# Kernel tuning notes

Measured on AMD Instinct MI355X. Metric: run time of the kernel, lower is better.

## Reference

```python
import jax, jax.numpy as jnp
import numpy as np

MIN_SCORE = 0.3       # min_score_threshold
NMS_THRESHOLD = 0.3   # nms_threshold
MAX_OUT = 256         # fixed output padding (jit-compatible replacement for dynamic K)


def _cxcywh_to_xyxy(b):
    cx, cy, w, h = b[..., 0], b[..., 1], b[..., 2], b[..., 3]
    half_w, half_h = w * 0.5, h * 0.5
    return jnp.stack([cx - half_w, cy - half_h, cx + half_w, cy + half_h], axis=-1)


def _pairwise_iou(a, b):
    # a: [N,4], b: [M,4] in xyxy
    lt = jnp.maximum(a[:, None, :2], b[None, :, :2])
    rb = jnp.minimum(a[:, None, 2:], b[None, :, 2:])
    wh = jnp.clip(rb - lt, 0.0)
    inter = wh[..., 0] * wh[..., 1]
    area_a = (a[:, 2] - a[:, 0]) * (a[:, 3] - a[:, 1])
    area_b = (b[:, 2] - b[:, 0]) * (b[:, 3] - b[:, 1])
    return inter / (area_a[:, None] + area_b[None, :] - inter + 1e-9)


def setup_inputs() -> dict:
    key = jax.random.key(0)
    k1, k2 = jax.random.split(key)
    N, n_coords = 8192, 16
    score = jax.random.uniform(k1, (N, 1), dtype=jnp.float32)
    box = jax.random.uniform(k2, (N, n_coords), dtype=jnp.float32)
    return {"score": score, "box": box}


def reference(score, box):
    # score: [N,1], box: [N,n_coords]; single class (n_classes==1, cls=None)
    s = score[:, 0]
    valid = s >= MIN_SCORE                      # score mask applied before NMS
    order = jnp.argsort(-s)                     # score-descending (batched_nms order)
    s_s = s[order]
    v_s = valid[order]
    box_s = box[order]
    bbox = _cxcywh_to_xyxy(box_s[:, :4]).astype(jnp.float32)
    iou = _pairwise_iou(bbox, bbox)             # [N,N]
    N = s.shape[0]

    def body(kept, i):
        # suppressed if overlaps any already-kept (higher-score) box
        suppressed = jnp.any(kept & (iou[:, i] > NMS_THRESHOLD))
        keep_i = v_s[i] & jnp.logical_not(suppressed)
        return kept.at[i].set(keep_i), None

    kept, _ = jax.lax.scan(body, jnp.zeros((N,), dtype=bool), jnp.arange(N))

    # compact kept detections to the front, preserving score order (stable sort)
    comp = jnp.argsort(jnp.where(kept, 0, 1), stable=True)[:MAX_OUT]
    out_valid = kept[comp]                      # [MAX_OUT]
    score_out = jnp.where(out_valid[:, None], s_s[comp][:, None], 0.0)   # [MAX_OUT,1]
    box_out = jnp.where(out_valid[:, None], box_s[comp], 0.0)            # [MAX_OUT,n_coords]
    return score_out, box_out, out_valid
```

## Files before the change

### kernel.cpp

```cpp
#include <hip/hip_runtime.h>
#include <stdint.h>

typedef unsigned long long u64;

#define N 8192
#define NW 128
#define MAX_OUT 256
#define MASK_BYTES ((size_t)N * NW * 8)


__global__ __launch_bounds__(256)
void build_keys_kernel(const float* __restrict__ score, u64* __restrict__ keys,
                       int* __restrict__ rank, int* __restrict__ nvalid) {
    int i = blockIdx.x * 256 + threadIdx.x;
    float s = score[i];
    uint32_t b = __float_as_uint(s);
    keys[i] = ((u64)(~b) << 32) | (uint32_t)i;
    rank[i] = 0;
    int c = (s >= 0.3f) ? 1 : 0;
    for (int off = 32; off; off >>= 1) c += __shfl_down(c, off);
    __shared__ int part[4];
    if ((threadIdx.x & 63) == 0) part[threadIdx.x >> 6] = c;
    __syncthreads();
    if (threadIdx.x == 0) atomicAdd(nvalid, part[0] + part[1] + part[2] + part[3]);
}

__global__ __launch_bounds__(256)
void rank_kernel(const u64* __restrict__ keys, int* __restrict__ rank) {
    __shared__ u64 kj[1024];
    const int tid = threadIdx.x;
    const int jbase = blockIdx.y * 1024;
    for (int t = tid; t < 1024; t += 256) kj[t] = keys[jbase + t];
    __syncthreads();
    const int i = blockIdx.x * 256 + tid;
    const u64 ki = keys[i];
    int c = 0;
    #pragma unroll 8
    for (int j = 0; j < 1024; ++j) c += (kj[j] < ki) ? 1 : 0;
    atomicAdd(&rank[i], c);
}

__global__ __launch_bounds__(256)
void scatter_kernel(const float* __restrict__ score, const float* __restrict__ box,
                    const int* __restrict__ rank, int* __restrict__ order,
                    float* __restrict__ s_s, float4* __restrict__ bbox,
                    float* __restrict__ area) {
    int i = blockIdx.x * 256 + threadIdx.x;
    int r = rank[i];
    float s = score[i];
    order[r] = i;
    s_s[r] = s;
    float4 cb = ((const float4*)box)[i * 4];
    float hw = cb.z * 0.5f, hh = cb.w * 0.5f;
    float x0 = cb.x - hw, y0 = cb.y - hh, x1 = cb.x + hw, y1 = cb.y + hh;
    bbox[r] = make_float4(x0, y0, x1, y1);
    area[r] = (x1 - x0) * (y1 - y0);
}

__global__ __launch_bounds__(256)
void mask_kernel(const float4* __restrict__ bbox, const float* __restrict__ area,
                 const int* __restrict__ nvalid_p, u64* __restrict__ mask) {
    const int w = blockIdx.x;
    const int i = blockIdx.y * 256 + threadIdx.x;
    __shared__ float4 jb[64];
    __shared__ float  ja[64];
    if (threadIdx.x < 64) {
        jb[threadIdx.x] = bbox[w * 64 + threadIdx.x];
        ja[threadIdx.x] = area[w * 64 + threadIdx.x];
    }
    __syncthreads();
    const int nv = *nvalid_p;
    if (i >= nv) return;
    if (w < (i >> 6)) return;
    float4 a = bbox[i];
    float  aa = area[i];
    u64 bits = 0;
    #pragma unroll 8
    for (int jj = 0; jj < 64; ++jj) {
        float4 b = jb[jj];
        float lx = fmaxf(a.x, b.x), ly = fmaxf(a.y, b.y);
        float rx = fminf(a.z, b.z), ry = fminf(a.w, b.w);
        float ww = fmaxf(rx - lx, 0.0f), hh = fmaxf(ry - ly, 0.0f);
        float inter = ww * hh;
        float denom = ((aa + ja[jj]) - inter) + 1e-9f;
        float iou = inter / denom;
        bits |= ((u64)(iou > 0.3f)) << jj;
    }
    mask[(size_t)i * NW + w] = bits;
}


struct Pipe { u64 col, s1, s2, g0, g1, g2, g3; };

__device__ __forceinline__ u64 wave_or64(u64 v) {
    unsigned lo = (unsigned)v, hi = (unsigned)(v >> 32);
    #pragma unroll
    for (int off = 1; off < 64; off <<= 1) {
        lo |= (unsigned)__shfl_xor((int)lo, off, 64);
        hi |= (unsigned)__shfl_xor((int)hi, off, 64);
    }
    return ((u64)hi << 32) | (u64)lo;
}

__global__ __launch_bounds__(64)
void nms_kernel(const u64* __restrict__ mask, const float* __restrict__ s_s,
                const int* __restrict__ order, const float* __restrict__ box,
                const int* __restrict__ nvalid_p, float* __restrict__ out) {
    const int lane = threadIdx.x;
    const int nv = *nvalid_p;
    const int nblk = (nv + 63) >> 6;
    __shared__ int kpos[MAX_OUT];
    int kcount = 0;
    u64 s1m = 0, s2m = 0, s2m_old = 0;

    Pipe A, B;
    A.col = A.s1 = A.s2 = A.g0 = A.g1 = A.g2 = A.g3 = 0;
    B.col = B.s1 = B.s2 = B.g0 = B.g1 = B.g2 = B.g3 = 0;
    if (nblk > 0) {
        const u64* r = mask + (size_t)lane * NW;
        A.col = r[0];
        if (nblk > 1) A.s1 = r[1];
        if (nblk > 2) A.s2 = r[2];
    }
    if (nblk > 1) {
        const u64* r = mask + (size_t)(64 + lane) * NW;
        B.col = r[1];
        if (nblk > 2) B.s1 = r[2];
        if (nblk > 3) B.s2 = r[3];
    }

    auto step = [&](int b, Pipe& P) -> bool {
        u64 col = P.col, s1v = P.s1, s2v = P.s2;
        u64 x = P.g0 | P.g1 | P.g2 | P.g3 | s1m | s2m_old;
        const int b2 = b + 2;
        P.col = P.s1 = P.s2 = P.g0 = P.g1 = P.g2 = P.g3 = 0;
        if (b2 < nblk) {
            const u64* r = mask + (size_t)((b2 << 6) + lane) * NW;
            P.col = r[b2];
            if (b2 + 1 < nblk) P.s1 = r[b2 + 1];
            if (b2 + 2 < nblk) P.s2 = r[b2 + 2];
            const int kc = kcount;
            if (lane < kc)       P.g0 = mask[(size_t)kpos[lane]       * NW + b2];
            if (lane +  64 < kc) P.g1 = mask[(size_t)kpos[lane +  64] * NW + b2];
            if (lane + 128 < kc) P.g2 = mask[(size_t)kpos[lane + 128] * NW + b2];
            if (lane + 192 < kc) P.g3 = mask[(size_t)kpos[lane + 192] * NW + b2];
        }
        u64 rw = wave_or64(x);
        const int base = b << 6;
        const int rem = nv - base;
        u64 validm = (rem >= 64) ? ~0ull : ((1ull << rem) - 1ull);
        u64 todo = validm & ~rw;
        u64 km = 0;
        while (todo) {
            int l = (int)__builtin_ctzll(todo);
            u64 row_l = __ballot(((col >> l) & 1ull) != 0);
            if (lane == 0) kpos[kcount] = base + l;
            km |= (1ull << l);
            kcount++;
            todo &= ~row_l;
            todo &= ~(1ull << l);
            if (kcount >= MAX_OUT) break;
        }
        u64 keepm = ((km >> lane) & 1ull) ? ~0ull : 0ull;
        s2m_old = s2m;
        s2m = s2v & keepm;
        s1m = s1v & keepm;
        return kcount < MAX_OUT;
    };

    bool run = true;
    for (int b = 0; run && b < nblk; b += 2) {
        run = step(b, A);
        if (run && b + 1 < nblk) run = step(b + 1, B);
    }

    __syncthreads();
    float* out_score = out;
    float* out_box   = out + MAX_OUT;
    float* out_valid = out + MAX_OUT + MAX_OUT * 16;
    const float4* box4 = (const float4*)box;
    float4* ob4 = (float4*)out_box;
    for (int t = lane; t < MAX_OUT; t += 64) {
        if (t < kcount) {
            int p = kpos[t];
            out_score[t] = s_s[p];
            out_valid[t] = 1.0f;
            int oi = order[p];
            #pragma unroll
            for (int q = 0; q < 4; ++q) ob4[t * 4 + q] = box4[oi * 4 + q];
        } else {
            out_score[t] = 0.0f;
            out_valid[t] = 0.0f;
            float4 z = make_float4(0.f, 0.f, 0.f, 0.f);
            #pragma unroll
            for (int q = 0; q < 4; ++q) ob4[t * 4 + q] = z;
        }
    }
}

extern "C" void kernel_launch(void* const* d_in, const int* in_sizes, int n_in,
                              void* d_out, int out_size, void* d_ws, size_t ws_size,
                              hipStream_t stream) {
    const float* score = (const float*)d_in[0];
    const float* box   = (const float*)d_in[1];
    char* ws = (char*)d_ws;
    u64*    mask   = (u64*)ws;
    u64*    keys   = (u64*)ws;
    int*    rank   = (int*)(ws + 65536);
    int*    order  = (int*)   (ws + MASK_BYTES);
    float*  s_s    = (float*) (ws + MASK_BYTES + 32768);
    float4* bbox   = (float4*)(ws + MASK_BYTES + 65536);
    float*  area   = (float*) (ws + MASK_BYTES + 65536 + 131072);
    int*    nvalid = (int*)   (ws + MASK_BYTES + 65536 + 131072 + 32768);

    hipMemsetAsync(nvalid, 0, sizeof(int), stream);
    build_keys_kernel<<<32, 256, 0, stream>>>(score, keys, rank, nvalid);
    rank_kernel<<<dim3(32, 8), 256, 0, stream>>>(keys, rank);
    scatter_kernel<<<32, 256, 0, stream>>>(score, box, rank, order, s_s, bbox, area);
    mask_kernel<<<dim3(128, 32), 256, 0, stream>>>(bbox, area, nvalid, mask);
    nms_kernel<<<1, 64, 0, stream>>>(mask, s_s, order, box, nvalid, (float*)d_out);
}
```

Before: 151.5 us.

## Track removal bitmap via kept-row loads instead of per-block column gathers

The NMS scan now accumulates a removal bitmap per lane: each lane holds two 64-bit words of the OR of kept rows. Suppression for a block comes from a shuffle broadcast of the owning lane's word, replacing the gather over all kept positions and the 64-lane OR reduction. Near-diagonal suppression is handled by broadcasting s1/s2 words of newly kept rows, and row loads are delayed through a three-slot rotation so they overlap later blocks. The nvalid count also moves from an atomic plus memset to per-block partials reduced inside the rank kernel, which drops one memset launch.

```diff
diff --git a/kernel.cpp b/kernel.cpp
--- a/kernel.cpp
+++ b/kernel.cpp
@@ -11,7 +11,7 @@
 
 __global__ __launch_bounds__(256)
 void build_keys_kernel(const float* __restrict__ score, u64* __restrict__ keys,
-                       int* __restrict__ rank, int* __restrict__ nvalid) {
+                       int* __restrict__ rank, int* __restrict__ partial) {
     int i = blockIdx.x * 256 + threadIdx.x;
     float s = score[i];
     uint32_t b = __float_as_uint(s);
@@ -22,13 +22,19 @@
     __shared__ int part[4];
     if ((threadIdx.x & 63) == 0) part[threadIdx.x >> 6] = c;
     __syncthreads();
-    if (threadIdx.x == 0) atomicAdd(nvalid, part[0] + part[1] + part[2] + part[3]);
-}
-
-__global__ __launch_bounds__(256)
-void rank_kernel(const u64* __restrict__ keys, int* __restrict__ rank) {
+    if (threadIdx.x == 0) partial[blockIdx.x] = part[0] + part[1] + part[2] + part[3];
+}
+
+__global__ __launch_bounds__(256)
+void rank_kernel(const u64* __restrict__ keys, int* __restrict__ rank,
+                 const int* __restrict__ partial, int* __restrict__ nvalid) {
     __shared__ u64 kj[1024];
     const int tid = threadIdx.x;
+    if (blockIdx.x == 0 && blockIdx.y == 0 && tid < 64) {
+        int v = (tid < 32) ? partial[tid] : 0;
+        for (int off = 32; off; off >>= 1) v += __shfl_down(v, off);
+        if (tid == 0) *nvalid = v;
+    }
     const int jbase = blockIdx.y * 1024;
     for (int t = tid; t < 1024; t += 256) kj[t] = keys[jbase + t];
     __syncthreads();
@@ -90,15 +96,12 @@
 }
 
 
-struct Pipe { u64 col, s1, s2, g0, g1, g2, g3; };
-
-__device__ __forceinline__ u64 wave_or64(u64 v) {
-    unsigned lo = (unsigned)v, hi = (unsigned)(v >> 32);
-    #pragma unroll
-    for (int off = 1; off < 64; off <<= 1) {
-        lo |= (unsigned)__shfl_xor((int)lo, off, 64);
-        hi |= (unsigned)__shfl_xor((int)hi, off, 64);
-    }
+struct Pipe { u64 col, s1, s2; };
+struct Rq   { u64 a0,b0,a1,b1,a2,b2,a3,b3; };
+
+__device__ __forceinline__ u64 bcast64(u64 v, int src) {
+    unsigned lo = (unsigned)__shfl((int)(unsigned)v, src);
+    unsigned hi = (unsigned)__shfl((int)(unsigned)(v >> 32), src);
     return ((u64)hi << 32) | (u64)lo;
 }
 
@@ -111,11 +114,12 @@
     const int nblk = (nv + 63) >> 6;
     __shared__ int kpos[MAX_OUT];
     int kcount = 0;
-    u64 s1m = 0, s2m = 0, s2m_old = 0;
-
-    Pipe A, B;
-    A.col = A.s1 = A.s2 = A.g0 = A.g1 = A.g2 = A.g3 = 0;
-    B.col = B.s1 = B.s2 = B.g0 = B.g1 = B.g2 = B.g3 = 0;
+    u64 remv0 = 0, remv1 = 0;
+    u64 rsup = 0;
+    u64 carry = 0;
+    Pipe A = {0,0,0}, B = {0,0,0};
+    Rq RA = {0,0,0,0,0,0,0,0}, RB = {0,0,0,0,0,0,0,0}, RC = {0,0,0,0,0,0,0,0};
+
     if (nblk > 0) {
         const u64* r = mask + (size_t)lane * NW;
         A.col = r[0];
@@ -129,27 +133,24 @@
         if (nblk > 3) B.s2 = r[3];
     }
 
-    auto step = [&](int b, Pipe& P) -> bool {
+    auto step = [&](int b, Pipe& P, Rq& R) -> bool {
+        remv0 |= R.a0 | R.a1 | R.a2 | R.a3;
+        remv1 |= R.b0 | R.b1 | R.b2 | R.b3;
+        u64 sel = (b & 1) ? remv1 : remv0;
+        u64 rw = bcast64(sel, b >> 1);
         u64 col = P.col, s1v = P.s1, s2v = P.s2;
-        u64 x = P.g0 | P.g1 | P.g2 | P.g3 | s1m | s2m_old;
         const int b2 = b + 2;
-        P.col = P.s1 = P.s2 = P.g0 = P.g1 = P.g2 = P.g3 = 0;
+        P.col = P.s1 = P.s2 = 0;
         if (b2 < nblk) {
             const u64* r = mask + (size_t)((b2 << 6) + lane) * NW;
             P.col = r[b2];
             if (b2 + 1 < nblk) P.s1 = r[b2 + 1];
             if (b2 + 2 < nblk) P.s2 = r[b2 + 2];
-            const int kc = kcount;
-            if (lane < kc)       P.g0 = mask[(size_t)kpos[lane]       * NW + b2];
-            if (lane +  64 < kc) P.g1 = mask[(size_t)kpos[lane +  64] * NW + b2];
-            if (lane + 128 < kc) P.g2 = mask[(size_t)kpos[lane + 128] * NW + b2];
-            if (lane + 192 < kc) P.g3 = mask[(size_t)kpos[lane + 192] * NW + b2];
-        }
-        u64 rw = wave_or64(x);
+        }
         const int base = b << 6;
         const int rem = nv - base;
         u64 validm = (rem >= 64) ? ~0ull : ((1ull << rem) - 1ull);
-        u64 todo = validm & ~rw;
+        u64 todo = validm & ~rw & ~rsup;
         u64 km = 0;
         while (todo) {
             int l = (int)__builtin_ctzll(todo);
@@ -161,17 +162,42 @@
             todo &= ~(1ull << l);
             if (kcount >= MAX_OUT) break;
         }
-        u64 keepm = ((km >> lane) & 1ull) ? ~0ull : 0ull;
-        s2m_old = s2m;
-        s2m = s2v & keepm;
-        s1m = s1v & keepm;
+        u64 add1 = 0, add2 = 0;
+        u64 t = km;
+        while (t) {
+            int l = (int)__builtin_ctzll(t); t &= t - 1;
+            add1 |= bcast64(s1v, l);
+            add2 |= bcast64(s2v, l);
+        }
+        rsup  = carry | add1;
+        carry = add2;
+        int l0 = -1, l1 = -1, l2 = -1, l3 = -1;
+        u64 t2 = km;
+        if (t2) { l0 = (int)__builtin_ctzll(t2); t2 &= t2 - 1; }
+        if (t2) { l1 = (int)__builtin_ctzll(t2); t2 &= t2 - 1; }
+        if (t2) { l2 = (int)__builtin_ctzll(t2); t2 &= t2 - 1; }
+        if (t2) { l3 = (int)__builtin_ctzll(t2); t2 &= t2 - 1; }
+        R.a0=R.b0=R.a1=R.b1=R.a2=R.b2=R.a3=R.b3 = 0;
+        if (l0 >= 0) { const u64* p = mask + (size_t)(base + l0) * NW + 2 * lane; R.a0 = p[0]; R.b0 = p[1]; }
+        if (l1 >= 0) { const u64* p = mask + (size_t)(base + l1) * NW + 2 * lane; R.a1 = p[0]; R.b1 = p[1]; }
+        if (l2 >= 0) { const u64* p = mask + (size_t)(base + l2) * NW + 2 * lane; R.a2 = p[0]; R.b2 = p[1]; }
+        if (l3 >= 0) { const u64* p = mask + (size_t)(base + l3) * NW + 2 * lane; R.a3 = p[0]; R.b3 = p[1]; }
+        while (t2) {
+            int l = (int)__builtin_ctzll(t2); t2 &= t2 - 1;
+            const u64* p = mask + (size_t)(base + l) * NW + 2 * lane;
+            remv0 |= p[0]; remv1 |= p[1];
+        }
         return kcount < MAX_OUT;
     };
 
     bool run = true;
-    for (int b = 0; run && b < nblk; b += 2) {
-        run = step(b, A);
-        if (run && b + 1 < nblk) run = step(b + 1, B);
+    for (int b = 0; run && b < nblk; b += 6) {
+        run = step(b, A, RA);
+        if (run && b + 1 < nblk) run = step(b + 1, B, RB);
+        if (run && b + 2 < nblk) run = step(b + 2, A, RC);
+        if (run && b + 3 < nblk) run = step(b + 3, B, RA);
+        if (run && b + 4 < nblk) run = step(b + 4, A, RB);
+        if (run && b + 5 < nblk) run = step(b + 5, B, RC);
     }
 
     __syncthreads();
@@ -204,18 +230,18 @@
     const float* score = (const float*)d_in[0];
     const float* box   = (const float*)d_in[1];
     char* ws = (char*)d_ws;
-    u64*    mask   = (u64*)ws;
-    u64*    keys   = (u64*)ws;
-    int*    rank   = (int*)(ws + 65536);
+    u64*    mask    = (u64*)ws;
+    u64*    keys    = (u64*)ws;
+    int*    rank    = (int*)(ws + 65536);
+    int*    partial = (int*)(ws + 98304);
     int*    order  = (int*)   (ws + MASK_BYTES);
     float*  s_s    = (float*) (ws + MASK_BYTES + 32768);
     float4* bbox   = (float4*)(ws + MASK_BYTES + 65536);
     float*  area   = (float*) (ws + MASK_BYTES + 65536 + 131072);
     int*    nvalid = (int*)   (ws + MASK_BYTES + 65536 + 131072 + 32768);
 
-    hipMemsetAsync(nvalid, 0, sizeof(int), stream);
-    build_keys_kernel<<<32, 256, 0, stream>>>(score, keys, rank, nvalid);
-    rank_kernel<<<dim3(32, 8), 256, 0, stream>>>(keys, rank);
+    build_keys_kernel<<<32, 256, 0, stream>>>(score, keys, rank, partial);
+    rank_kernel<<<dim3(32, 8), 256, 0, stream>>>(keys, rank, partial, nvalid);
     scatter_kernel<<<32, 256, 0, stream>>>(score, box, rank, order, s_s, bbox, area);
     mask_kernel<<<dim3(128, 32), 256, 0, stream>>>(bbox, area, nvalid, mask);
     nms_kernel<<<1, 64, 0, stream>>>(mask, s_s, order, box, nvalid, (float*)d_out);
```

New measurement: 212.5 us. +40.3%, slower.
